# Kernel optimization log

Hardware: AMD Instinct MI355X
Metric: run time of the kernel (lower is better)

## Reference

```python
import jax, jax.numpy as jnp
import numpy as np

N = 50000      # nodes
E = 1_600_000  # edges (avg degree 32)
IN, H, OUT, R = 128, 64, 32, 8
NEG_SLOPE = 0.2


def _rgat(x, src, dst, etype, W, q, k, b, n_nodes):
    """PyG RGATConv, defaults: heads=1, dim=1, additive-self-attention,
    across-relation softmax, concat=True, bias=True, dropout=0 (eval)."""
    # per-relation transform of all nodes: [R, N, O] (cheaper than per-edge bmm since 2*deg >> R)
    t = jnp.einsum('ni,rio->rno', x, W)
    xi = t[etype, dst]                      # [E, O] transformed target feats
    xj = t[etype, src]                      # [E, O] transformed source feats
    a = (xi @ q + xj @ k)[:, 0]             # [E] additive attention logits
    a = jnp.where(a >= 0, a, NEG_SLOPE * a)  # leaky_relu
    # segment softmax over incoming edges of each target node (across relations)
    m = jax.ops.segment_max(a, dst, num_segments=n_nodes)
    m = jnp.where(jnp.isfinite(m), m, 0.0)
    ex = jnp.exp(a - m[dst])
    s = jax.ops.segment_sum(ex, dst, num_segments=n_nodes)
    alpha = ex / (s[dst] + 1e-16)
    out = jax.ops.segment_sum(alpha[:, None] * xj, dst, num_segments=n_nodes)
    return out + b


def setup_inputs() -> dict:
    key = jax.random.key(0)
    ks = jax.random.split(key, 24)
    x = jax.random.normal(ks[0], (N, IN), jnp.float32)
    edge_index = jax.random.randint(ks[1], (2, E), 0, N, jnp.int32)
    edge_type = jax.random.randint(ks[2], (E,), 0, R, jnp.int32)

    def glorot(k, shape, fan_in):
        return jax.random.normal(k, shape, jnp.float32) * (1.0 / np.sqrt(fan_in))

    d = dict(x=x, edge_index=edge_index, edge_type=edge_type)
    # conv1: in->hidden, conv_mu / conv_logvar: hidden->hidden
    d['W1'] = glorot(ks[3], (R, IN, H), IN)
    d['q1'] = glorot(ks[4], (H, 1), H)
    d['k1'] = glorot(ks[5], (H, 1), H)
    d['b1'] = jnp.zeros((H,), jnp.float32)
    d['Wmu'] = glorot(ks[6], (R, H, H), H)
    d['qmu'] = glorot(ks[7], (H, 1), H)
    d['kmu'] = glorot(ks[8], (H, 1), H)
    d['bmu'] = jnp.zeros((H,), jnp.float32)
    d['Wlv'] = glorot(ks[9], (R, H, H), H)
    d['qlv'] = glorot(ks[10], (H, 1), H)
    d['klv'] = glorot(ks[11], (H, 1), H)
    d['blv'] = jnp.zeros((H,), jnp.float32)
    d['Wm'] = glorot(ks[12], (H, OUT), H)   # linear_mu (stored [in,out])
    d['bm'] = jnp.zeros((OUT,), jnp.float32)
    d['Wl'] = glorot(ks[13], (H, OUT), H)   # linear_logvar
    d['bl'] = jnp.zeros((OUT,), jnp.float32)
    return d


def reference(x, edge_index, edge_type, W1, q1, k1, b1,
              Wmu, qmu, kmu, bmu, Wlv, qlv, klv, blv, Wm, bm, Wl, bl):
    src, dst = edge_index[0], edge_index[1]
    hidden = jax.nn.relu(_rgat(x, src, dst, edge_type, W1, q1, k1, b1, N))
    mu = jax.nn.relu(_rgat(hidden, src, dst, edge_type, Wmu, qmu, kmu, bmu, N))
    mu = mu @ Wm + bm                       # dropout is identity in eval
    logvar = jax.nn.relu(_rgat(hidden, src, dst, edge_type, Wlv, qlv, klv, blv, N))
    logvar = logvar @ Wl + bl
    logstd = 0.5 * logvar
    return (mu, logstd)
```

## Files before the change

### kernel.cpp

```cpp
#include <hip/hip_runtime.h>
#include <cstdint>

#define HDIM 64
#define ODIM 32
#define NEG_SLOPE 0.2f
#define SCHUNK 2048
#define EPB 8192

typedef __attribute__((ext_vector_type(8))) short v8s;
typedef __attribute__((ext_vector_type(4))) float v4f;

__device__ __forceinline__ unsigned f2bf_rne(float f) {
  unsigned u = __float_as_uint(f);
  return (u + 0x7FFFu + ((u >> 16) & 1u)) >> 16;
}

__device__ __forceinline__ unsigned fenc(float f) {
  unsigned u = __float_as_uint(f);
  return (u & 0x80000000u) ? ~u : (u | 0x80000000u);
}
__device__ __forceinline__ float fdec(unsigned e) {
  unsigned u = (e & 0x80000000u) ? (e ^ 0x80000000u) : ~e;
  return __uint_as_float(u);
}

__global__ __launch_bounds__(256) void cvt_bf16_kernel(
    const float* __restrict__ in, unsigned short* __restrict__ out, int n) {
  int i = (blockIdx.x * 256 + threadIdx.x) * 4;
  if (i + 3 < n) {
    float4 v = *(const float4*)&in[i];
    ushort4 o;
    o.x = (unsigned short)f2bf_rne(v.x);
    o.y = (unsigned short)f2bf_rne(v.y);
    o.z = (unsigned short)f2bf_rne(v.z);
    o.w = (unsigned short)f2bf_rne(v.w);
    *(ushort4*)&out[i] = o;
  }
}

__global__ __launch_bounds__(256) void transpose_w_kernel(
    const float* __restrict__ W1, const float* __restrict__ Wmu,
    const float* __restrict__ Wlv, unsigned short* __restrict__ W1t,
    unsigned short* __restrict__ Wct) {
  const int b = blockIdx.x;
  if (b < 8) {
    const int r = b;
    for (int idx = threadIdx.x; idx < 128 * 64; idx += 256) {
      const int kk = idx >> 6, o = idx & 63;
      W1t[((size_t)r * 64 + o) * 128 + kk] =
          (unsigned short)f2bf_rne(W1[((size_t)r * 128 + kk) * 64 + o]);
    }
  } else {
    const int s = (b - 8) >> 3, r = (b - 8) & 7;
    const float* src = s ? Wlv : Wmu;
    for (int idx = threadIdx.x; idx < 64 * 64; idx += 256) {
      const int kk = idx >> 6, o = idx & 63;
      Wct[((size_t)s * 64 + o) * 512 + r * 64 + kk] =
          (unsigned short)f2bf_rne(src[((size_t)r * 64 + kk) * 64 + o]);
    }
  }
}

__global__ __launch_bounds__(256) void prep_T_kernel(
    const float* __restrict__ Wmu, const float* __restrict__ qmu,
    const float* __restrict__ kmu, const float* __restrict__ Wlv,
    const float* __restrict__ qlv, const float* __restrict__ klv,
    float* __restrict__ T) {
  for (int idx = threadIdx.x; idx < 2048; idx += 256) {
    const int j = idx >> 6, c = idx & 63;
    const int isk = j >> 4, sr = j & 15, s = sr >> 3, r = sr & 7;
    const float* W = s ? Wlv : Wmu;
    const float* vec = s ? (isk ? klv : qlv) : (isk ? kmu : qmu);
    float acc = 0.f;
    for (int o = 0; o < 64; o++)
      acc += W[((size_t)r * 64 + c) * 64 + o] * vec[o];
    T[idx] = acc;
  }
}

__global__ __launch_bounds__(256) void count_deg_kernel(
    const int* __restrict__ dst, const int* __restrict__ etype,
    int* __restrict__ deg, int E) {
  int e = blockIdx.x * 256 + threadIdx.x;
  if (e < E) atomicAdd(&deg[dst[e] * 8 + etype[e]], 1);
}

__global__ __launch_bounds__(256) void scan_p1(const int* __restrict__ deg,
                                               int* __restrict__ bsum, int n) {
  int base = blockIdx.x * SCHUNK + threadIdx.x * 8;
  int s = 0;
#pragma unroll
  for (int j = 0; j < 8; j++) {
    int i = base + j;
    if (i < n) s += deg[i];
  }
#pragma unroll
  for (int d = 1; d < 64; d <<= 1) s += __shfl_xor(s, d, 64);
  __shared__ int ws[4];
  if ((threadIdx.x & 63) == 0) ws[threadIdx.x >> 6] = s;
  __syncthreads();
  if (threadIdx.x == 0) bsum[blockIdx.x] = ws[0] + ws[1] + ws[2] + ws[3];
}

__global__ __launch_bounds__(256) void scan_p2(int* bsum, int nb) {
  __shared__ int wsum[4];
  const int i = threadIdx.x;
  int v = (i < nb) ? bsum[i] : 0;
  const int orig = v;
  const int lane = i & 63, w = i >> 6;
#pragma unroll
  for (int d = 1; d < 64; d <<= 1) {
    int up = __shfl_up(v, d, 64);
    if (lane >= d) v += up;
  }
  if (lane == 63) wsum[w] = v;
  __syncthreads();
  int woff = 0;
#pragma unroll
  for (int k = 0; k < 4; k++) woff += (k < w) ? wsum[k] : 0;
  if (i < nb) bsum[i] = woff + v - orig;
}

__global__ __launch_bounds__(256) void scan_p3(const int* __restrict__ deg,
                                               const int* __restrict__ bsum,
                                               int* __restrict__ row_ptr,
                                               int n) {
  int base = blockIdx.x * SCHUNK + threadIdx.x * 8;
  int vals[8];
  int s = 0;
#pragma unroll
  for (int j = 0; j < 8; j++) {
    int i = base + j;
    vals[j] = (i < n) ? deg[i] : 0;
    s += vals[j];
  }
  int lane = threadIdx.x & 63, w = threadIdx.x >> 6;
  int v = s;
#pragma unroll
  for (int d = 1; d < 64; d <<= 1) {
    int up = __shfl_up(v, d, 64);
    if (lane >= d) v += up;
  }
  __shared__ int wsum[4];
  if (lane == 63) wsum[w] = v;
  __syncthreads();
  int woff = 0;
#pragma unroll
  for (int i = 0; i < 4; i++) woff += (i < w) ? wsum[i] : 0;
  int off = bsum[blockIdx.x] + woff + v - s;
#pragma unroll
  for (int j = 0; j < 8; j++) {
    int i = base + j;
    off += vals[j];
    if (i < n) row_ptr[i + 1] = off;
  }
  if (blockIdx.x == 0 && threadIdx.x == 0) row_ptr[0] = 0;
}

__global__ __launch_bounds__(256) void bucket_cursor_init(
    const int* __restrict__ rp2, int* __restrict__ cursor, int N, int nb) {
  int i = threadIdx.x;
  if (i < nb) cursor[i] = rp2[(size_t)min(i * 256, N) * 8];
}

__global__ __launch_bounds__(256) void bucket_pass1(
    const int* __restrict__ src, const int* __restrict__ dst,
    const int* __restrict__ etype, int* __restrict__ cursor,
    unsigned* __restrict__ tmp, int E) {
  __shared__ int hist[256];
  __shared__ int binstart[256];
  __shared__ int gbase[256];
  __shared__ int fill[256];
  __shared__ int wsum[4];
  __shared__ unsigned stage[EPB];
  __shared__ unsigned char binof[EPB];
  const int tid = threadIdx.x;
  const int e0 = blockIdx.x * EPB;
  const int cnt = min(EPB, E - e0);

  hist[tid] = 0;
  fill[tid] = 0;
  __syncthreads();
  for (int j = tid; j < cnt; j += 256) atomicAdd(&hist[dst[e0 + j] >> 8], 1);
  __syncthreads();

  const int hv = hist[tid];
  {
    const int lane = tid & 63, w = tid >> 6;
    int iv = hv;
#pragma unroll
    for (int d = 1; d < 64; d <<= 1) {
      int up = __shfl_up(iv, d, 64);
      if (lane >= d) iv += up;
    }
    if (lane == 63) wsum[w] = iv;
    __syncthreads();
    int woff = 0;
#pragma unroll
    for (int i = 0; i < 4; i++) woff += (i < w) ? wsum[i] : 0;
    binstart[tid] = woff + iv - hv;
    if (hv > 0) gbase[tid] = atomicAdd(&cursor[tid], hv);
  }
  __syncthreads();

  for (int j = tid; j < cnt; j += 256) {
    const int d = dst[e0 + j];
    const int b = d >> 8;
    const unsigned rec = ((unsigned)(d & 255) << 19) |
                         ((unsigned)etype[e0 + j] << 16) |
                         (unsigned)src[e0 + j];
    const int slot = binstart[b] + atomicAdd(&fill[b], 1);
    stage[slot] = rec;
    binof[slot] = (unsigned char)b;
  }
  __syncthreads();

  for (int s = tid; s < cnt; s += 256) {
    const int b = binof[s];
    tmp[gbase[b] + (s - binstart[b])] = stage[s];
  }
}

__global__ __launch_bounds__(256) void bucket_pass2(
    const int* __restrict__ rp2, const unsigned* __restrict__ tmp,
    int* __restrict__ edges, int N) {
  __shared__ int rp[2049];
  __shared__ int fill[2048];
  const int tid = threadIdx.x;
  const int rowbase = blockIdx.x * 256;
  const int rowcnt = min(256, N - rowbase);
  for (int i = tid; i <= rowcnt * 8; i += 256) rp[i] = rp2[(size_t)rowbase * 8 + i];
  for (int i = tid; i < 2048; i += 256) fill[i] = 0;
  __syncthreads();
  const int beg = rp[0];
  const int endv = rp[rowcnt * 8];
  for (int i = beg + tid; i < endv; i += 256) {
    const unsigned rec = tmp[i];
    const int bin = rec >> 16;
    const int pos = rp[bin] + atomicAdd(&fill[bin], 1);
    edges[pos] = (int)(rec & 0x7FFFFu);
  }
}

__global__ __launch_bounds__(256) void rowmax_kernel(
    const float* __restrict__ ak, unsigned* __restrict__ maxk_enc, int N) {
  const int row = blockIdx.x;
  const int nchunks = gridDim.y;
  const int per = (N + nchunks - 1) / nchunks;
  const int beg = blockIdx.y * per;
  const int end = min(N, beg + per);
  const float* r = ak + (size_t)row * N;
  float m = -1e30f;
  for (int i = beg + threadIdx.x; i < end; i += 256) m = fmaxf(m, r[i]);
#pragma unroll
  for (int d = 1; d < 64; d <<= 1) m = fmaxf(m, __shfl_xor(m, d, 64));
  __shared__ float ws[4];
  if ((threadIdx.x & 63) == 0) ws[threadIdx.x >> 6] = m;
  __syncthreads();
  if (threadIdx.x == 0) {
    float bm = fmaxf(fmaxf(ws[0], ws[1]), fmaxf(ws[2], ws[3]));
    atomicMax(&maxk_enc[row], fenc(bm));
  }
}

__global__ __launch_bounds__(256) void transform1_mfma(
    const unsigned short* __restrict__ xb,
    const unsigned short* __restrict__ W1t, const float* __restrict__ q,
    const float* __restrict__ k, unsigned short* __restrict__ tb,
    float* __restrict__ aq, float* __restrict__ ak, int N) {
  __shared__ unsigned short st[4][16][72];
  const int r = blockIdx.x;
  const int tid = threadIdx.x;
  const int w = tid >> 6;
  const int lane = tid & 63;
  const int quad = lane >> 4;
  const int mrow = lane & 15;
  const int n0w = blockIdx.y * 64 + w * 16;

  const int gA = min(n0w + mrow, N - 1);
  const unsigned short* arow = xb + (size_t)gA * 128 + quad * 8;
  const unsigned short* wrow = W1t + ((size_t)r * 64 + mrow) * 128 + quad * 8;

  v4f acc[4];
#pragma unroll
  for (int tt = 0; tt < 4; tt++) acc[tt] = (v4f){0.f, 0.f, 0.f, 0.f};

#pragma unroll
  for (int k0 = 0; k0 < 128; k0 += 32) {
    v8s a = *(const v8s*)(arow + k0);
#pragma unroll
    for (int tt = 0; tt < 4; tt++) {
      v8s b = *(const v8s*)(wrow + (size_t)tt * 16 * 128 + k0);
      acc[tt] = __builtin_amdgcn_mfma_f32_16x16x32_bf16(a, b, acc[tt], 0, 0, 0);
    }
  }

  float qv[4], kv[4];
#pragma unroll
  for (int tt = 0; tt < 4; tt++) {
    qv[tt] = q[tt * 16 + mrow];
    kv[tt] = k[tt * 16 + mrow];
  }

#pragma unroll
  for (int i = 0; i < 4; i++) {
    float vq = 0.f, vk = 0.f;
#pragma unroll
    for (int tt = 0; tt < 4; tt++) {
      vq = fmaf(acc[tt][i], qv[tt], vq);
      vk = fmaf(acc[tt][i], kv[tt], vk);
      st[w][quad * 4 + i][tt * 16 + mrow] =
          (unsigned short)f2bf_rne(acc[tt][i]);
    }
#pragma unroll
    for (int d = 1; d < 16; d <<= 1) {
      vq += __shfl_xor(vq, d, 64);
      vk += __shfl_xor(vk, d, 64);
    }
    const int gn = n0w + quad * 4 + i;
    if (mrow == 0 && gn < N) {
      aq[(size_t)r * N + gn] = vq;
      ak[(size_t)r * N + gn] = vk;
    }
  }
  __syncthreads();

  const int row = lane >> 2, cg = lane & 3;
  const int gns = n0w + row;
  if (gns < N) {
    const uint4 v0 = *(const uint4*)&st[w][row][cg * 16];
    const uint4 v1 = *(const uint4*)&st[w][row][cg * 16 + 8];
    uint4* dst = (uint4*)&tb[((size_t)r * N + gns) * 64 + cg * 16];
    dst[0] = v0;
    dst[1] = v1;
  }
}

__global__ __launch_bounds__(256) void aggregate_kernel(
    const int* __restrict__ rp2, const int* __restrict__ edges,
    const unsigned short* __restrict__ tb, const float* __restrict__ aq,
    const float* __restrict__ ak, const unsigned* __restrict__ maxk_enc,
    const float* __restrict__ bias, unsigned short* __restrict__ hb, int N) {
  const int tid = threadIdx.x;
  const int w = tid >> 6, o = tid & 63;
  int wid = blockIdx.x * 4 + w;
  const bool valid = wid < N;
  if (!valid) wid = N - 1;
  const int beg = rp2[(size_t)wid * 8];
  const int end = valid ? rp2[(size_t)wid * 8 + 8] : beg;
  const int deg = end - beg;

  const float aqw = aq[(size_t)(o & 7) * N + wid];

  float v = aqw + fdec(maxk_enc[o & 7]);
  v = (v >= 0.f) ? v : NEG_SLOPE * v;
#pragma unroll
  for (int d = 1; d < 8; d <<= 1) v = fmaxf(v, __shfl_xor(v, d, 64));
  const float m = __shfl(v, 0, 64);

  const int g = o >> 3;
  const int cl = o & 7;
  float s = 0.f;
  float acc[8];
#pragma unroll
  for (int c = 0; c < 8; c++) acc[c] = 0.f;

  for (int base = 0; base < deg; base += 64) {
    const int j = base + o;
    const int gcount = min(64, deg - base);
    const int packed = edges[beg + min(j, deg - 1)];
    const int src = packed & 0xFFFF;
    const int rr = packed >> 16;
    const int idx = rr * N + src;
    float x = __shfl(aqw, rr, 64) + ak[idx];
    x = (x >= 0.f) ? x : NEG_SLOPE * x;
    const float p = (j < deg) ? __expf(x - m) : 0.f;
    s += p;
    const int g8 = (gcount + 7) & ~7;
    for (int u = 0; u < g8; u += 8) {
      const int e = u + g;
      const float pe = __shfl(p, e, 64);
      const int ie = __shfl(idx, e, 64);
      const uint4 tv = *(const uint4*)(tb + (size_t)ie * 64 + cl * 8);
      const unsigned uu0 = tv.x, uu1 = tv.y, uu2 = tv.z, uu3 = tv.w;
      acc[0] = fmaf(pe, __uint_as_float(uu0 << 16), acc[0]);
      acc[1] = fmaf(pe, __uint_as_float(uu0 & 0xFFFF0000u), acc[1]);
      acc[2] = fmaf(pe, __uint_as_float(uu1 << 16), acc[2]);
      acc[3] = fmaf(pe, __uint_as_float(uu1 & 0xFFFF0000u), acc[3]);
      acc[4] = fmaf(pe, __uint_as_float(uu2 << 16), acc[4]);
      acc[5] = fmaf(pe, __uint_as_float(uu2 & 0xFFFF0000u), acc[5]);
      acc[6] = fmaf(pe, __uint_as_float(uu3 << 16), acc[6]);
      acc[7] = fmaf(pe, __uint_as_float(uu3 & 0xFFFF0000u), acc[7]);
    }
  }
#pragma unroll
  for (int d = 1; d < 64; d <<= 1) s += __shfl_xor(s, d, 64);
#pragma unroll
  for (int d = 8; d < 64; d <<= 1) {
#pragma unroll
    for (int c = 0; c < 8; c++) acc[c] += __shfl_xor(acc[c], d, 64);
  }

  if (valid && g == 0) {
    const float inv = 1.f / (s + 1e-16f);
    unsigned rv[8];
#pragma unroll
    for (int c = 0; c < 8; c++) {
      const float res = acc[c] * inv + bias[cl * 8 + c];
      rv[c] = f2bf_rne(fmaxf(res, 0.f));
    }
    uint4 pkd;
    pkd.x = rv[0] | (rv[1] << 16);
    pkd.y = rv[2] | (rv[3] << 16);
    pkd.z = rv[4] | (rv[5] << 16);
    pkd.w = rv[6] | (rv[7] << 16);
    *(uint4*)(hb + (size_t)wid * 64 + cl * 8) = pkd;
  }
}

__global__ __launch_bounds__(256) void logit2_kernel(
    const unsigned short* __restrict__ hb, const float* __restrict__ T,
    float* __restrict__ aq2, float* __restrict__ ak2, int N) {
  __shared__ float Ts[2048];
  for (int i = threadIdx.x; i < 2048; i += 256) Ts[i] = T[i];
  __syncthreads();
  const int n = blockIdx.x * 256 + threadIdx.x;
  if (n >= N) return;
  float h[64];
  const unsigned short* hr = hb + (size_t)n * 64;
#pragma unroll
  for (int d = 0; d < 8; d++) {
    const uint4 u = *(const uint4*)(hr + d * 8);
    h[d * 8 + 0] = __uint_as_float(u.x << 16);
    h[d * 8 + 1] = __uint_as_float(u.x & 0xFFFF0000u);
    h[d * 8 + 2] = __uint_as_float(u.y << 16);
    h[d * 8 + 3] = __uint_as_float(u.y & 0xFFFF0000u);
    h[d * 8 + 4] = __uint_as_float(u.z << 16);
    h[d * 8 + 5] = __uint_as_float(u.z & 0xFFFF0000u);
    h[d * 8 + 6] = __uint_as_float(u.w << 16);
    h[d * 8 + 7] = __uint_as_float(u.w & 0xFFFF0000u);
  }
#pragma unroll
  for (int j = 0; j < 16; j++) {
    float dq = 0.f, dk = 0.f;
#pragma unroll
    for (int c = 0; c < 64; c++) {
      dq = fmaf(h[c], Ts[j * 64 + c], dq);
      dk = fmaf(h[c], Ts[(16 + j) * 64 + c], dk);
    }
    aq2[(size_t)j * N + n] = dq;
    ak2[(size_t)j * N + n] = dk;
  }
}

__global__ __launch_bounds__(256) void aggregate2h_kernel(
    const int* __restrict__ rp2, const int* __restrict__ edges,
    const unsigned short* __restrict__ hb, const float* __restrict__ aq2,
    const float* __restrict__ ak2, const unsigned* __restrict__ maxk2_enc,
    unsigned* __restrict__ y, float* __restrict__ sbuf, int N) {
  __shared__ float sred[2][2];
  const int tid = threadIdx.x;
  const int w = tid >> 6, o = tid & 63;
  const int nl = w >> 1;
  const int rbase = (w & 1) * 4;
  int wid = blockIdx.x * 2 + nl;
  const bool valid = wid < N;
  if (!valid) wid = N - 1;
  if (tid < 4) ((float*)sred)[tid] = 0.f;
  __syncthreads();

  const float aqw = aq2[(size_t)(o & 15) * N + wid];
  float v = aqw + fdec(maxk2_enc[o & 15]);
  v = (v >= 0.f) ? v : NEG_SLOPE * v;
#pragma unroll
  for (int d = 1; d < 8; d <<= 1) v = fmaxf(v, __shfl_xor(v, d, 64));
  const float m0 = __shfl(v, 0, 64);
  const float m1 = __shfl(v, 8, 64);

  const int g = o >> 5;
  const int k = o & 31;
  float s0 = 0.f, s1 = 0.f;
  float aE0[4], aO0[4], aE1[4], aO1[4];
#pragma unroll
  for (int r = 0; r < 4; r++) {
    aE0[r] = 0.f;
    aO0[r] = 0.f;
    aE1[r] = 0.f;
    aO1[r] = 0.f;
  }

  const size_t segbase = (size_t)wid * 8 + rbase;
#pragma unroll
  for (int r = 0; r < 4; r++) {
    const int sb = rp2[segbase + r];
    const int se = rp2[segbase + r + 1];
    if (valid && sb < se) {
      const float aqr0 = __shfl(aqw, rbase + r, 64);
      const float aqr1 = __shfl(aqw, 8 + rbase + r, 64);
      for (int base = sb; base < se; base += 64) {
        const int j = base + o;
        const int cnt = min(64, se - base);
        const int src = edges[min(j, se - 1)] & 0xFFFF;
        const float akv0 = ak2[(size_t)(rbase + r) * N + src];
        const float akv1 = ak2[(size_t)(8 + rbase + r) * N + src];
        float x0 = aqr0 + akv0;
        float x1 = aqr1 + akv1;
        x0 = (x0 >= 0.f) ? x0 : NEG_SLOPE * x0;
        x1 = (x1 >= 0.f) ? x1 : NEG_SLOPE * x1;
        const float p0 = (j < se) ? __expf(x0 - m0) : 0.f;
        const float p1 = (j < se) ? __expf(x1 - m1) : 0.f;
        s0 += p0;
        s1 += p1;
        for (int u = 0; 2 * u < cnt; u++) {
          const int e = 2 * u + g;
          const float pe0 = __shfl(p0, e, 64);
          const float pe1 = __shfl(p1, e, 64);
          const int ie = __shfl(src, e, 64);
          const unsigned hw =
              *(const unsigned*)(hb + (size_t)ie * 64 + k * 2);
          const float h0 = __uint_as_float(hw << 16);
          const float h1 = __uint_as_float(hw & 0xFFFF0000u);
          aE0[r] = fmaf(pe0, h0, aE0[r]);
          aO0[r] = fmaf(pe0, h1, aO0[r]);
          aE1[r] = fmaf(pe1, h0, aE1[r]);
          aO1[r] = fmaf(pe1, h1, aO1[r]);
        }
      }
    }
  }

#pragma unroll
  for (int d = 1; d < 64; d <<= 1) {
    s0 += __shfl_xor(s0, d, 64);
    s1 += __shfl_xor(s1, d, 64);
  }
#pragma unroll
  for (int r = 0; r < 4; r++) {
    aE0[r] += __shfl_xor(aE0[r], 32, 64);
    aO0[r] += __shfl_xor(aO0[r], 32, 64);
    aE1[r] += __shfl_xor(aE1[r], 32, 64);
    aO1[r] += __shfl_xor(aO1[r], 32, 64);
  }
  if (valid && o == 0) {
    atomicAdd(&sred[nl][0], s0);
    atomicAdd(&sred[nl][1], s1);
  }
  if (valid && g == 0) {
#pragma unroll
    for (int r = 0; r < 4; r++) {
      const unsigned u0 = f2bf_rne(aE0[r]) | (f2bf_rne(aO0[r]) << 16);
      const unsigned u1 = f2bf_rne(aE1[r]) | (f2bf_rne(aO1[r]) << 16);
      y[(size_t)wid * 256 + (rbase + r) * 32 + k] = u0;
      y[((size_t)N + wid) * 256 + (rbase + r) * 32 + k] = u1;
    }
  }
  __syncthreads();
  if (valid && o == 0 && rbase == 0) {
    sbuf[(size_t)wid * 2 + 0] = sred[nl][0];
    sbuf[(size_t)wid * 2 + 1] = sred[nl][1];
  }
}

__global__ __launch_bounds__(256) void out2_kernel(
    const unsigned short* __restrict__ yb,
    const unsigned short* __restrict__ Wct, const float* __restrict__ sbuf,
    const float* __restrict__ bmu, const float* __restrict__ blv,
    const float* __restrict__ Wm, const float* __restrict__ bm,
    const float* __restrict__ Wl, const float* __restrict__ bl,
    float* __restrict__ out_mu, float* __restrict__ out_ls, int N) {
  __shared__ float hstf[64][65];
  __shared__ float WL[2048];
  __shared__ float b2L[32];
  const int s = blockIdx.y;
  const int tid = threadIdx.x;
  for (int i = tid; i < 2048; i += 256) WL[i] = s ? Wl[i] : Wm[i];
  if (tid < 32) b2L[tid] = s ? bl[tid] : bm[tid];

  const int w = tid >> 6, lane = tid & 63;
  const int quad = lane >> 4, mrow = lane & 15;
  const int n0w = blockIdx.x * 64 + w * 16;
  const int gA = min(n0w + mrow, N - 1);
  const unsigned short* arow = yb + ((size_t)s * N + gA) * 512 + quad * 8;
  const unsigned short* wrow = Wct + ((size_t)s * 64 + mrow) * 512 + quad * 8;

  v4f acc[4];
#pragma unroll
  for (int tt = 0; tt < 4; tt++) acc[tt] = (v4f){0.f, 0.f, 0.f, 0.f};
#pragma unroll
  for (int k0 = 0; k0 < 512; k0 += 32) {
    v8s a = *(const v8s*)(arow + k0);
#pragma unroll
    for (int tt = 0; tt < 4; tt++) {
      v8s b = *(const v8s*)(wrow + (size_t)tt * 16 * 512 + k0);
      acc[tt] = __builtin_amdgcn_mfma_f32_16x16x32_bf16(a, b, acc[tt], 0, 0, 0);
    }
  }

  const float* bc = s ? blv : bmu;
#pragma unroll
  for (int i = 0; i < 4; i++) {
    const int node = min(n0w + quad * 4 + i, N - 1);
    const float inv = 1.f / (sbuf[(size_t)node * 2 + s] + 1e-16f);
#pragma unroll
    for (int tt = 0; tt < 4; tt++) {
      hstf[w * 16 + quad * 4 + i][tt * 16 + mrow] =
          fmaxf(acc[tt][i] * inv + bc[tt * 16 + mrow], 0.f);
    }
  }
  __syncthreads();

  const float mul = s ? 0.5f : 1.f;
  float* outp = s ? out_ls : out_mu;
  for (int idx = tid; idx < 2048; idx += 256) {
    const int nl2 = idx >> 5, oo = idx & 31;
    const int node = blockIdx.x * 64 + nl2;
    float a2 = 0.f;
#pragma unroll
    for (int c = 0; c < 64; c++) a2 = fmaf(hstf[nl2][c], WL[c * 32 + oo], a2);
    if (node < N) outp[(size_t)node * 32 + oo] = (a2 + b2L[oo]) * mul;
  }
}

extern "C" void kernel_launch(void* const* d_in, const int* in_sizes, int n_in,
                              void* d_out, int out_size, void* d_ws,
                              size_t ws_size, hipStream_t stream) {
  const float* x = (const float*)d_in[0];
  const int* edge_index = (const int*)d_in[1];
  const int* edge_type = (const int*)d_in[2];
  const float* W1 = (const float*)d_in[3];
  const float* q1 = (const float*)d_in[4];
  const float* k1 = (const float*)d_in[5];
  const float* b1 = (const float*)d_in[6];
  const float* Wmu = (const float*)d_in[7];
  const float* qmu = (const float*)d_in[8];
  const float* kmu = (const float*)d_in[9];
  const float* bmu = (const float*)d_in[10];
  const float* Wlv = (const float*)d_in[11];
  const float* qlv = (const float*)d_in[12];
  const float* klv = (const float*)d_in[13];
  const float* blv = (const float*)d_in[14];
  const float* Wm = (const float*)d_in[15];
  const float* bm = (const float*)d_in[16];
  const float* Wl = (const float*)d_in[17];
  const float* bl = (const float*)d_in[18];

  const int N = in_sizes[0] / 128;
  const int E = in_sizes[2];
  const int R = in_sizes[3] / (128 * 64);

  float* out_mu = (float*)d_out;
  float* out_ls = (float*)d_out + (size_t)N * ODIM;

  char* wsp = (char*)d_ws;
  size_t off = 0;
  auto carve = [&](size_t bytes) {
    void* p = wsp + off;
    off += (bytes + 255) & ~(size_t)255;
    return p;
  };

  void* tbuf = carve((size_t)R * N * 64 * sizeof(unsigned));
  unsigned short* t1b = (unsigned short*)tbuf;
  unsigned short* yb = (unsigned short*)tbuf;
  unsigned* yw = (unsigned*)tbuf;
  unsigned short* xb = (unsigned short*)carve((size_t)N * 128 * 2);
  unsigned short* hb = (unsigned short*)carve((size_t)N * 64 * 2);
  unsigned short* W1t = (unsigned short*)carve((size_t)R * 64 * 128 * 2);
  unsigned short* Wct = (unsigned short*)carve((size_t)2 * 64 * 512 * 2);
  float* Tdir = (float*)carve((size_t)32 * 64 * sizeof(float));
  float* aq2 = (float*)carve((size_t)2 * R * N * sizeof(float));
  float* ak2 = (float*)carve((size_t)2 * R * N * sizeof(float));
  unsigned* maxk_enc = (unsigned*)carve(2 * R * sizeof(unsigned));
  float* sbuf = (float*)carve((size_t)N * 2 * sizeof(float));
  int* deg = (int*)carve((size_t)N * 8 * sizeof(int));
  int* rp2 = (int*)carve(((size_t)N * 8 + 1) * sizeof(int));
  int* bsum = (int*)carve(256 * sizeof(int));
  int* cursor = (int*)carve(256 * sizeof(int));
  unsigned* tmp = (unsigned*)carve((size_t)E * sizeof(unsigned));
  int* edges = (int*)carve((size_t)E * sizeof(int));

  const int* e_src = edge_index;
  const int* e_dst = edge_index + E;

  cvt_bf16_kernel<<<(N * 128 / 4 + 255) / 256, 256, 0, stream>>>(x, xb,
                                                                 N * 128);
  transpose_w_kernel<<<24, 256, 0, stream>>>(W1, Wmu, Wlv, W1t, Wct);
  prep_T_kernel<<<1, 256, 0, stream>>>(Wmu, qmu, kmu, Wlv, qlv, klv, Tdir);

  hipMemsetAsync(deg, 0, (size_t)N * 8 * sizeof(int), stream);
  hipMemsetAsync(maxk_enc, 0, 2 * R * sizeof(unsigned), stream);
  count_deg_kernel<<<(E + 255) / 256, 256, 0, stream>>>(e_dst, edge_type, deg,
                                                        E);
  const int n2 = N * 8;
  const int nchunk = (n2 + SCHUNK - 1) / SCHUNK;
  scan_p1<<<nchunk, 256, 0, stream>>>(deg, bsum, n2);
  scan_p2<<<1, 256, 0, stream>>>(bsum, nchunk);
  scan_p3<<<nchunk, 256, 0, stream>>>(deg, bsum, rp2, n2);

  const int nbuck = (N + 255) >> 8;
  bucket_cursor_init<<<1, 256, 0, stream>>>(rp2, cursor, N, nbuck);
  bucket_pass1<<<(E + EPB - 1) / EPB, 256, 0, stream>>>(e_src, e_dst,
                                                        edge_type, cursor,
                                                        tmp, E);
  bucket_pass2<<<nbuck, 256, 0, stream>>>(rp2, tmp, edges, N);

  const int nb64 = (N + 63) / 64;

  transform1_mfma<<<dim3(R, nb64), 256, 0, stream>>>(xb, W1t, q1, k1, t1b,
                                                     aq2, ak2, N);
  rowmax_kernel<<<dim3(R, 32), 256, 0, stream>>>(ak2, maxk_enc, N);
  aggregate_kernel<<<(N + 3) / 4, 256, 0, stream>>>(rp2, edges, t1b, aq2, ak2,
                                                    maxk_enc, b1, hb, N);

  logit2_kernel<<<(N + 255) / 256, 256, 0, stream>>>(hb, Tdir, aq2, ak2, N);
  hipMemsetAsync(maxk_enc, 0, 2 * R * sizeof(unsigned), stream);
  rowmax_kernel<<<dim3(2 * R, 32), 256, 0, stream>>>(ak2, maxk_enc, N);
  aggregate2h_kernel<<<(N + 1) / 2, 256, 0, stream>>>(rp2, edges, hb, aq2,
                                                      ak2, maxk_enc, yw, sbuf,
                                                      N);
  out2_kernel<<<dim3(nb64, 2), 256, 0, stream>>>(yb, Wct, sbuf, bmu, blv, Wm,
                                                 bm, Wl, bl, out_mu, out_ls,
                                                 N);
}
```

Before: 609.4 us.

## Build node-level CSR, fuse key max into logit kernels, LDS-atomic aggregation

Replaces the per-(node, relation) CSR with a node-only CSR, which shrinks the degree count, the scan and the bucket pass. Relation types travel packed in the edge records instead. The per-relation key max is now computed inside transform1 and logit2 using wave reductions plus atomicMax, which removes the separate rowmax kernels and one memset. aggregate2h now gives each wave one whole node and accumulates per-relation sums in LDS with float atomicAdd on a swizzled layout, in place of register accumulators per relation segment. This can add LDS atomic contention on the second-layer aggregation in exchange for fewer passes and better balanced work.

After: 1.602 ms. 163% more time.

```diff
diff --git a/kernel.cpp b/kernel.cpp
--- a/kernel.cpp
+++ b/kernel.cpp
@@ -79,10 +79,9 @@
 }
 
 __global__ __launch_bounds__(256) void count_deg_kernel(
-    const int* __restrict__ dst, const int* __restrict__ etype,
-    int* __restrict__ deg, int E) {
+    const int* __restrict__ dst, int* __restrict__ deg, int E) {
   int e = blockIdx.x * 256 + threadIdx.x;
-  if (e < E) atomicAdd(&deg[dst[e] * 8 + etype[e]], 1);
+  if (e < E) atomicAdd(&deg[dst[e]], 1);
 }
 
 __global__ __launch_bounds__(256) void scan_p1(const int* __restrict__ deg,
@@ -102,23 +101,16 @@
   if (threadIdx.x == 0) bsum[blockIdx.x] = ws[0] + ws[1] + ws[2] + ws[3];
 }
 
-__global__ __launch_bounds__(256) void scan_p2(int* bsum, int nb) {
-  __shared__ int wsum[4];
-  const int i = threadIdx.x;
+__global__ void scan_p2(int* bsum, int nb) {
+  int i = threadIdx.x;
   int v = (i < nb) ? bsum[i] : 0;
-  const int orig = v;
-  const int lane = i & 63, w = i >> 6;
+  int orig = v;
 #pragma unroll
   for (int d = 1; d < 64; d <<= 1) {
     int up = __shfl_up(v, d, 64);
-    if (lane >= d) v += up;
-  }
-  if (lane == 63) wsum[w] = v;
-  __syncthreads();
-  int woff = 0;
-#pragma unroll
-  for (int k = 0; k < 4; k++) woff += (k < w) ? wsum[k] : 0;
-  if (i < nb) bsum[i] = woff + v - orig;
+    if (i >= d) v += up;
+  }
+  if (i < nb) bsum[i] = v - orig;
 }
 
 __global__ __launch_bounds__(256) void scan_p3(const int* __restrict__ deg,
@@ -158,9 +150,9 @@
 }
 
 __global__ __launch_bounds__(256) void bucket_cursor_init(
-    const int* __restrict__ rp2, int* __restrict__ cursor, int N, int nb) {
+    const int* __restrict__ row_ptr, int* __restrict__ cursor, int N, int nb) {
   int i = threadIdx.x;
-  if (i < nb) cursor[i] = rp2[(size_t)min(i * 256, N) * 8];
+  if (i < nb) cursor[i] = row_ptr[min(i * 256, N)];
 }
 
 __global__ __launch_bounds__(256) void bucket_pass1(
@@ -222,44 +214,23 @@
 }
 
 __global__ __launch_bounds__(256) void bucket_pass2(
-    const int* __restrict__ rp2, const unsigned* __restrict__ tmp,
+    const int* __restrict__ row_ptr, const unsigned* __restrict__ tmp,
     int* __restrict__ edges, int N) {
-  __shared__ int rp[2049];
-  __shared__ int fill[2048];
+  __shared__ int rp[257];
+  __shared__ int fill[256];
   const int tid = threadIdx.x;
   const int rowbase = blockIdx.x * 256;
   const int rowcnt = min(256, N - rowbase);
-  for (int i = tid; i <= rowcnt * 8; i += 256) rp[i] = rp2[(size_t)rowbase * 8 + i];
-  for (int i = tid; i < 2048; i += 256) fill[i] = 0;
+  for (int i = tid; i <= rowcnt; i += 256) rp[i] = row_ptr[rowbase + i];
+  fill[tid] = 0;
   __syncthreads();
   const int beg = rp[0];
-  const int endv = rp[rowcnt * 8];
+  const int endv = rp[rowcnt];
   for (int i = beg + tid; i < endv; i += 256) {
     const unsigned rec = tmp[i];
-    const int bin = rec >> 16;
-    const int pos = rp[bin] + atomicAdd(&fill[bin], 1);
+    const int dlow = rec >> 19;
+    const int pos = rp[dlow] + atomicAdd(&fill[dlow], 1);
     edges[pos] = (int)(rec & 0x7FFFFu);
-  }
-}
-
-__global__ __launch_bounds__(256) void rowmax_kernel(
-    const float* __restrict__ ak, unsigned* __restrict__ maxk_enc, int N) {
-  const int row = blockIdx.x;
-  const int nchunks = gridDim.y;
-  const int per = (N + nchunks - 1) / nchunks;
-  const int beg = blockIdx.y * per;
-  const int end = min(N, beg + per);
-  const float* r = ak + (size_t)row * N;
-  float m = -1e30f;
-  for (int i = beg + threadIdx.x; i < end; i += 256) m = fmaxf(m, r[i]);
-#pragma unroll
-  for (int d = 1; d < 64; d <<= 1) m = fmaxf(m, __shfl_xor(m, d, 64));
-  __shared__ float ws[4];
-  if ((threadIdx.x & 63) == 0) ws[threadIdx.x >> 6] = m;
-  __syncthreads();
-  if (threadIdx.x == 0) {
-    float bm = fmaxf(fmaxf(ws[0], ws[1]), fmaxf(ws[2], ws[3]));
-    atomicMax(&maxk_enc[row], fenc(bm));
   }
 }
 
@@ -267,8 +238,10 @@
     const unsigned short* __restrict__ xb,
     const unsigned short* __restrict__ W1t, const float* __restrict__ q,
     const float* __restrict__ k, unsigned short* __restrict__ tb,
-    float* __restrict__ aq, float* __restrict__ ak, int N) {
+    float* __restrict__ aq, float* __restrict__ ak,
+    unsigned* __restrict__ maxk_enc, int N) {
   __shared__ unsigned short st[4][16][72];
+  __shared__ float wsm[4];
   const int r = blockIdx.x;
   const int tid = threadIdx.x;
   const int w = tid >> 6;
@@ -302,6 +275,7 @@
     kv[tt] = k[tt * 16 + mrow];
   }
 
+  float kmax = -1e30f;
 #pragma unroll
   for (int i = 0; i < 4; i++) {
     float vq = 0.f, vk = 0.f;
@@ -317,13 +291,21 @@
       vq += __shfl_xor(vq, d, 64);
       vk += __shfl_xor(vk, d, 64);
     }
+    kmax = fmaxf(kmax, vk);
     const int gn = n0w + quad * 4 + i;
     if (mrow == 0 && gn < N) {
       aq[(size_t)r * N + gn] = vq;
       ak[(size_t)r * N + gn] = vk;
     }
   }
-  __syncthreads();
+#pragma unroll
+  for (int d = 1; d < 64; d <<= 1) kmax = fmaxf(kmax, __shfl_xor(kmax, d, 64));
+  if (lane == 0) wsm[w] = kmax;
+  __syncthreads();
+  if (tid == 0) {
+    atomicMax(&maxk_enc[r],
+              fenc(fmaxf(fmaxf(wsm[0], wsm[1]), fmaxf(wsm[2], wsm[3]))));
+  }
 
   const int row = lane >> 2, cg = lane & 3;
   const int gns = n0w + row;
@@ -337,7 +319,7 @@
 }
 
 __global__ __launch_bounds__(256) void aggregate_kernel(
-    const int* __restrict__ rp2, const int* __restrict__ edges,
+    const int* __restrict__ row_ptr, const int* __restrict__ edges,
     const unsigned short* __restrict__ tb, const float* __restrict__ aq,
     const float* __restrict__ ak, const unsigned* __restrict__ maxk_enc,
     const float* __restrict__ bias, unsigned short* __restrict__ hb, int N) {
@@ -346,8 +328,8 @@
   int wid = blockIdx.x * 4 + w;
   const bool valid = wid < N;
   if (!valid) wid = N - 1;
-  const int beg = rp2[(size_t)wid * 8];
-  const int end = valid ? rp2[(size_t)wid * 8 + 8] : beg;
+  const int beg = row_ptr[wid];
+  const int end = valid ? row_ptr[wid + 1] : beg;
   const int deg = end - beg;
 
   const float aqw = aq[(size_t)(o & 7) * N + wid];
@@ -420,12 +402,15 @@
 
 __global__ __launch_bounds__(256) void logit2_kernel(
     const unsigned short* __restrict__ hb, const float* __restrict__ T,
-    float* __restrict__ aq2, float* __restrict__ ak2, int N) {
+    float* __restrict__ aq2, float* __restrict__ ak2,
+    unsigned* __restrict__ maxk2_enc, int N) {
   __shared__ float Ts[2048];
+  __shared__ float wred[4][16];
   for (int i = threadIdx.x; i < 2048; i += 256) Ts[i] = T[i];
   __syncthreads();
-  const int n = blockIdx.x * 256 + threadIdx.x;
-  if (n >= N) return;
+  const int n0 = blockIdx.x * 256 + threadIdx.x;
+  const bool valid = n0 < N;
+  const int n = valid ? n0 : N - 1;
   float h[64];
   const unsigned short* hr = hb + (size_t)n * 64;
 #pragma unroll
@@ -440,6 +425,7 @@
     h[d * 8 + 6] = __uint_as_float(u.w << 16);
     h[d * 8 + 7] = __uint_as_float(u.w & 0xFFFF0000u);
   }
+  float kmx[16];
 #pragma unroll
   for (int j = 0; j < 16; j++) {
     float dq = 0.f, dk = 0.f;
@@ -448,26 +434,48 @@
       dq = fmaf(h[c], Ts[j * 64 + c], dq);
       dk = fmaf(h[c], Ts[(16 + j) * 64 + c], dk);
     }
-    aq2[(size_t)j * N + n] = dq;
-    ak2[(size_t)j * N + n] = dk;
+    if (valid) {
+      aq2[(size_t)j * N + n] = dq;
+      ak2[(size_t)j * N + n] = dk;
+    }
+    kmx[j] = dk;
+  }
+  const int lane = threadIdx.x & 63, w = threadIdx.x >> 6;
+#pragma unroll
+  for (int j = 0; j < 16; j++) {
+#pragma unroll
+    for (int d = 1; d < 64; d <<= 1)
+      kmx[j] = fmaxf(kmx[j], __shfl_xor(kmx[j], d, 64));
+    if (lane == 0) wred[w][j] = kmx[j];
+  }
+  __syncthreads();
+  if (threadIdx.x < 16) {
+    const float bm = fmaxf(fmaxf(wred[0][threadIdx.x], wred[1][threadIdx.x]),
+                           fmaxf(wred[2][threadIdx.x], wred[3][threadIdx.x]));
+    atomicMax(&maxk2_enc[threadIdx.x], fenc(bm));
   }
 }
 
 __global__ __launch_bounds__(256) void aggregate2h_kernel(
-    const int* __restrict__ rp2, const int* __restrict__ edges,
+    const int* __restrict__ row_ptr, const int* __restrict__ edges,
     const unsigned short* __restrict__ hb, const float* __restrict__ aq2,
     const float* __restrict__ ak2, const unsigned* __restrict__ maxk2_enc,
     unsigned* __restrict__ y, float* __restrict__ sbuf, int N) {
-  __shared__ float sred[2][2];
+  __shared__ float y0s[4][512];
+  __shared__ float y1s[4][512];
   const int tid = threadIdx.x;
   const int w = tid >> 6, o = tid & 63;
-  const int nl = w >> 1;
-  const int rbase = (w & 1) * 4;
-  int wid = blockIdx.x * 2 + nl;
+  for (int i = o; i < 512; i += 64) {
+    y0s[w][i] = 0.f;
+    y1s[w][i] = 0.f;
+  }
+
+  int wid = blockIdx.x * 4 + w;
   const bool valid = wid < N;
   if (!valid) wid = N - 1;
-  if (tid < 4) ((float*)sred)[tid] = 0.f;
-  __syncthreads();
+  const int beg = row_ptr[wid];
+  const int end = valid ? row_ptr[wid + 1] : beg;
+  const int deg = end - beg;
 
   const float aqw = aq2[(size_t)(o & 15) * N + wid];
   float v = aqw + fdec(maxk2_enc[o & 15]);
@@ -477,87 +485,72 @@
   const float m0 = __shfl(v, 0, 64);
   const float m1 = __shfl(v, 8, 64);
 
-  const int g = o >> 5;
-  const int k = o & 31;
+  const int g = o >> 4;
+  const int cl = o & 15;
   float s0 = 0.f, s1 = 0.f;
-  float aE0[4], aO0[4], aE1[4], aO1[4];
-#pragma unroll
-  for (int r = 0; r < 4; r++) {
-    aE0[r] = 0.f;
-    aO0[r] = 0.f;
-    aE1[r] = 0.f;
-    aO1[r] = 0.f;
-  }
-
-  const size_t segbase = (size_t)wid * 8 + rbase;
-#pragma unroll
-  for (int r = 0; r < 4; r++) {
-    const int sb = rp2[segbase + r];
-    const int se = rp2[segbase + r + 1];
-    if (valid && sb < se) {
-      const float aqr0 = __shfl(aqw, rbase + r, 64);
-      const float aqr1 = __shfl(aqw, 8 + rbase + r, 64);
-      for (int base = sb; base < se; base += 64) {
-        const int j = base + o;
-        const int cnt = min(64, se - base);
-        const int src = edges[min(j, se - 1)] & 0xFFFF;
-        const float akv0 = ak2[(size_t)(rbase + r) * N + src];
-        const float akv1 = ak2[(size_t)(8 + rbase + r) * N + src];
-        float x0 = aqr0 + akv0;
-        float x1 = aqr1 + akv1;
-        x0 = (x0 >= 0.f) ? x0 : NEG_SLOPE * x0;
-        x1 = (x1 >= 0.f) ? x1 : NEG_SLOPE * x1;
-        const float p0 = (j < se) ? __expf(x0 - m0) : 0.f;
-        const float p1 = (j < se) ? __expf(x1 - m1) : 0.f;
-        s0 += p0;
-        s1 += p1;
-        for (int u = 0; 2 * u < cnt; u++) {
-          const int e = 2 * u + g;
-          const float pe0 = __shfl(p0, e, 64);
-          const float pe1 = __shfl(p1, e, 64);
-          const int ie = __shfl(src, e, 64);
-          const unsigned hw =
-              *(const unsigned*)(hb + (size_t)ie * 64 + k * 2);
-          const float h0 = __uint_as_float(hw << 16);
-          const float h1 = __uint_as_float(hw & 0xFFFF0000u);
-          aE0[r] = fmaf(pe0, h0, aE0[r]);
-          aO0[r] = fmaf(pe0, h1, aO0[r]);
-          aE1[r] = fmaf(pe1, h0, aE1[r]);
-          aO1[r] = fmaf(pe1, h1, aO1[r]);
-        }
-      }
-    }
-  }
-
+
+  for (int base = 0; base < deg; base += 64) {
+    const int j = base + o;
+    const int gcount = min(64, deg - base);
+    const int packed = edges[beg + min(j, deg - 1)];
+    const int src = packed & 0xFFFF;
+    const int rr = packed >> 16;
+    const int idx = rr * N + src;
+    float x0 = __shfl(aqw, rr, 64) + ak2[idx];
+    float x1 = __shfl(aqw, 8 + rr, 64) + ak2[idx + 8 * N];
+    x0 = (x0 >= 0.f) ? x0 : NEG_SLOPE * x0;
+    x1 = (x1 >= 0.f) ? x1 : NEG_SLOPE * x1;
+    const float p0 = (j < deg) ? __expf(x0 - m0) : 0.f;
+    const float p1 = (j < deg) ? __expf(x1 - m1) : 0.f;
+    s0 += p0;
+    s1 += p1;
+    const int g4 = (gcount + 3) & ~3;
+    for (int u = 0; u < g4; u += 4) {
+      const int e = u + g;
+      const float pe0 = __shfl(p0, e, 64);
+      const float pe1 = __shfl(p1, e, 64);
+      const int pk = __shfl(packed, e, 64);
+      const int se_ = pk & 0xFFFF;
+      const int re_ = pk >> 16;
+      const uint2 hw = *(const uint2*)(hb + (size_t)se_ * 64 + cl * 4);
+      const float h0 = __uint_as_float(hw.x << 16);
+      const float h1 = __uint_as_float(hw.x & 0xFFFF0000u);
+      const float h2 = __uint_as_float(hw.y << 16);
+      const float h3 = __uint_as_float(hw.y & 0xFFFF0000u);
+      const int bse = re_ * 64 + ((cl * 4 + re_ * 8) & 63);
+      float* Y0 = &y0s[w][bse];
+      float* Y1 = &y1s[w][bse];
+      atomicAdd(&Y0[0], pe0 * h0);
+      atomicAdd(&Y0[1], pe0 * h1);
+      atomicAdd(&Y0[2], pe0 * h2);
+      atomicAdd(&Y0[3], pe0 * h3);
+      atomicAdd(&Y1[0], pe1 * h0);
+      atomicAdd(&Y1[1], pe1 * h1);
+      atomicAdd(&Y1[2], pe1 * h2);
+      atomicAdd(&Y1[3], pe1 * h3);
+    }
+  }
 #pragma unroll
   for (int d = 1; d < 64; d <<= 1) {
     s0 += __shfl_xor(s0, d, 64);
     s1 += __shfl_xor(s1, d, 64);
   }
-#pragma unroll
-  for (int r = 0; r < 4; r++) {
-    aE0[r] += __shfl_xor(aE0[r], 32, 64);
-    aO0[r] += __shfl_xor(aO0[r], 32, 64);
-    aE1[r] += __shfl_xor(aE1[r], 32, 64);
-    aO1[r] += __shfl_xor(aO1[r], 32, 64);
-  }
-  if (valid && o == 0) {
-    atomicAdd(&sred[nl][0], s0);
-    atomicAdd(&sred[nl][1], s1);
-  }
-  if (valid && g == 0) {
-#pragma unroll
-    for (int r = 0; r < 4; r++) {
-      const unsigned u0 = f2bf_rne(aE0[r]) | (f2bf_rne(aO0[r]) << 16);
-      const unsigned u1 = f2bf_rne(aE1[r]) | (f2bf_rne(aO1[r]) << 16);
-      y[(size_t)wid * 256 + (rbase + r) * 32 + k] = u0;
-      y[((size_t)N + wid) * 256 + (rbase + r) * 32 + k] = u1;
-    }
-  }
-  __syncthreads();
-  if (valid && o == 0 && rbase == 0) {
-    sbuf[(size_t)wid * 2 + 0] = sred[nl][0];
-    sbuf[(size_t)wid * 2 + 1] = sred[nl][1];
+
+  if (valid) {
+    const float* Y = (o < 32) ? y0s[w] : y1s[w];
+    const int k = o & 31;
+    const size_t nb_ = ((size_t)((o < 32) ? 0 : N) + wid) * 256;
+#pragma unroll
+    for (int rr = 0; rr < 8; rr++) {
+      const int c0 = (2 * k + rr * 8) & 63;
+      const float a0 = Y[rr * 64 + c0];
+      const float a1 = Y[rr * 64 + c0 + 1];
+      y[nb_ + rr * 32 + k] = f2bf_rne(a0) | (f2bf_rne(a1) << 16);
+    }
+    if (o == 0) {
+      sbuf[(size_t)wid * 2 + 0] = s0;
+      sbuf[(size_t)wid * 2 + 1] = s1;
+    }
   }
 }
 
@@ -670,10 +663,10 @@
   float* Tdir = (float*)carve((size_t)32 * 64 * sizeof(float));
   float* aq2 = (float*)carve((size_t)2 * R * N * sizeof(float));
   float* ak2 = (float*)carve((size_t)2 * R * N * sizeof(float));
-  unsigned* maxk_enc = (unsigned*)carve(2 * R * sizeof(unsigned));
+  unsigned* maxk_enc = (unsigned*)carve(32 * sizeof(unsigned));
   float* sbuf = (float*)carve((size_t)N * 2 * sizeof(float));
-  int* deg = (int*)carve((size_t)N * 8 * sizeof(int));
-  int* rp2 = (int*)carve(((size_t)N * 8 + 1) * sizeof(int));
+  int* deg = (int*)carve((size_t)N * sizeof(int));
+  int* row_ptr = (int*)carve((size_t)(N + 1) * sizeof(int));
   int* bsum = (int*)carve(256 * sizeof(int));
   int* cursor = (int*)carve(256 * sizeof(int));
   unsigned* tmp = (unsigned*)carve((size_t)E * sizeof(unsigned));
@@ -687,37 +680,33 @@
   transpose_w_kernel<<<24, 256, 0, stream>>>(W1, Wmu, Wlv, W1t, Wct);
   prep_T_kernel<<<1, 256, 0, stream>>>(Wmu, qmu, kmu, Wlv, qlv, klv, Tdir);
 
-  hipMemsetAsync(deg, 0, (size_t)N * 8 * sizeof(int), stream);
-  hipMemsetAsync(maxk_enc, 0, 2 * R * sizeof(unsigned), stream);
-  count_deg_kernel<<<(E + 255) / 256, 256, 0, stream>>>(e_dst, edge_type, deg,
-                                                        E);
-  const int n2 = N * 8;
-  const int nchunk = (n2 + SCHUNK - 1) / SCHUNK;
-  scan_p1<<<nchunk, 256, 0, stream>>>(deg, bsum, n2);
-  scan_p2<<<1, 256, 0, stream>>>(bsum, nchunk);
-  scan_p3<<<nchunk, 256, 0, stream>>>(deg, bsum, rp2, n2);
+  hipMemsetAsync(deg, 0, (size_t)N * sizeof(int), stream);
+  hipMemsetAsync(maxk_enc, 0, 32 * sizeof(unsigned), stream);
+  count_deg_kernel<<<(E + 255) / 256, 256, 0, stream>>>(e_dst, deg, E);
+  const int nchunk = (N + SCHUNK - 1) / SCHUNK;
+  scan_p1<<<nchunk, 256, 0, stream>>>(deg, bsum, N);
+  scan_p2<<<1, 64, 0, stream>>>(bsum, nchunk);
+  scan_p3<<<nchunk, 256, 0, stream>>>(deg, bsum, row_ptr, N);
 
   const int nbuck = (N + 255) >> 8;
-  bucket_cursor_init<<<1, 256, 0, stream>>>(rp2, cursor, N, nbuck);
+  bucket_cursor_init<<<1, 256, 0, stream>>>(row_ptr, cursor, N, nbuck);
   bucket_pass1<<<(E + EPB - 1) / EPB, 256, 0, stream>>>(e_src, e_dst,
                                                         edge_type, cursor,
                                                         tmp, E);
-  bucket_pass2<<<nbuck, 256, 0, stream>>>(rp2, tmp, edges, N);
+  bucket_pass2<<<nbuck, 256, 0, stream>>>(row_ptr, tmp, edges, N);
 
   const int nb64 = (N + 63) / 64;
+  const int agg_blocks = (N + 3) / 4;
 
   transform1_mfma<<<dim3(R, nb64), 256, 0, stream>>>(xb, W1t, q1, k1, t1b,
-                                                     aq2, ak2, N);
-  rowmax_kernel<<<dim3(R, 32), 256, 0, stream>>>(ak2, maxk_enc, N);
-  aggregate_kernel<<<(N + 3) / 4, 256, 0, stream>>>(rp2, edges, t1b, aq2, ak2,
-                                                    maxk_enc, b1, hb, N);
-
-  logit2_kernel<<<(N + 255) / 256, 256, 0, stream>>>(hb, Tdir, aq2, ak2, N);
-  hipMemsetAsync(maxk_enc, 0, 2 * R * sizeof(unsigned), stream);
-  rowmax_kernel<<<dim3(2 * R, 32), 256, 0, stream>>>(ak2, maxk_enc, N);
-  aggregate2h_kernel<<<(N + 1) / 2, 256, 0, stream>>>(rp2, edges, hb, aq2,
-                                                      ak2, maxk_enc, yw, sbuf,
-                                                      N);
+                                                     aq2, ak2, maxk_enc, N);
+  aggregate_kernel<<<agg_blocks, 256, 0, stream>>>(
+      row_ptr, edges, t1b, aq2, ak2, maxk_enc, b1, hb, N);
+
+  logit2_kernel<<<(N + 255) / 256, 256, 0, stream>>>(hb, Tdir, aq2, ak2,
+                                                     maxk_enc + 8, N);
+  aggregate2h_kernel<<<agg_blocks, 256, 0, stream>>>(
+      row_ptr, edges, hb, aq2, ak2, maxk_enc + 8, yw, sbuf, N);
   out2_kernel<<<dim3(nb64, 2), 256, 0, stream>>>(yb, Wct, sbuf, bmu, blv, Wm,
                                                  bm, Wl, bl, out_mu, out_ls,
                                                  N);
```
